# Kernel optimization log

Hardware: AMD Instinct MI355X
Metric: run time of the kernel (lower is better)

Reference implementation:

```python
import jax, jax.numpy as jnp
import numpy as np
import math

N_LAYERS = 6
F = 512   # num_feature
H = 8     # num_head
DH = F // H
V = 32000 # vocab size
B = 64
S = 512   # == PositionalEncoding max_len
EPS = 1e-5


def _make_pe(max_len, d_model):
    position = np.arange(max_len, dtype=np.float32)[:, None]
    div_term = np.exp(np.arange(0, d_model, 2, dtype=np.float32) * (-math.log(10000.0) / d_model))
    pe = np.zeros((max_len, d_model), dtype=np.float32)
    pe[:, 0::2] = np.sin(position * div_term)
    pe[:, 1::2] = np.cos(position * div_term)
    return jnp.asarray(pe)


def setup_inputs() -> dict:
    key = jax.random.key(0)
    ks = jax.random.split(key, 16)
    w = lambda k, shape, s=0.02: (jax.random.normal(k, shape, dtype=jnp.float32) * s)
    inp = {
        "text": jax.random.randint(ks[0], (B, S), 0, V),
        "emb": jax.random.normal(ks[1], (V, F), dtype=jnp.float32) * 0.25,
        "pe": _make_pe(S, F),
        # per-layer params stacked on leading N axis
        "Wq": w(ks[2], (N_LAYERS, F, F)), "bq": jnp.zeros((N_LAYERS, F), jnp.float32),
        "Wk": w(ks[3], (N_LAYERS, F, F)), "bk": jnp.zeros((N_LAYERS, F), jnp.float32),
        "Wv": w(ks[4], (N_LAYERS, F, F)), "bv": jnp.zeros((N_LAYERS, F), jnp.float32),
        "g1": jnp.ones((N_LAYERS, F), jnp.float32), "beta1": jnp.zeros((N_LAYERS, F), jnp.float32),
        "Wf": w(ks[5], (N_LAYERS, F, F)), "bf": jnp.zeros((N_LAYERS, F), jnp.float32),
        "g2": jnp.ones((N_LAYERS, F), jnp.float32), "beta2": jnp.zeros((N_LAYERS, F), jnp.float32),
    }
    return inp


def _layernorm(x, g, b):
    m = jnp.mean(x, axis=-1, keepdims=True)
    v = jnp.mean(jnp.square(x - m), axis=-1, keepdims=True)
    return (x - m) * jax.lax.rsqrt(v + EPS) * g + b


def _encoder_layer(x, Wq, bq, Wk, bk, Wv, bv, g1, beta1, Wf, bf, g2, beta2):
    Bz, Sz, Fz = x.shape
    q = (x @ Wq + bq).reshape(Bz, Sz, H, DH)
    k = (x @ Wk + bk).reshape(Bz, Sz, H, DH)
    v = (x @ Wv + bv).reshape(Bz, Sz, H, DH)
    # FAITHFUL to source bug: attention over HEADS per token, no 1/sqrt(d) scaling.
    score = jnp.einsum('bshd,bsgd->bshg', q, k)          # [B,S,H,H]
    weight = jax.nn.softmax(score, axis=-1)
    attn = jnp.einsum('bshg,bsgd->bshd', weight, v).reshape(Bz, Sz, Fz)
    x = _layernorm(attn + x, g1, beta1)
    x = _layernorm((x @ Wf + bf) + x, g2, beta2)
    return x


def reference(text, emb, pe, Wq, bq, Wk, bk, Wv, bv, g1, beta1, Wf, bf, g2, beta2):
    x = emb[text] + pe[None, :text.shape[1], :]  # embedding + pos-enc (dropout = eval identity)
    for i in range(N_LAYERS):
        x = _encoder_layer(x, Wq[i], bq[i], Wk[i], bk[i], Wv[i], bv[i],
                           g1[i], beta1[i], Wf[i], bf[i], g2[i], beta2[i])
    return x
```

## Files before the change

### kernel.cpp

```cpp
#include <hip/hip_runtime.h>
#include <stdint.h>

typedef unsigned short u16;
using frag8 = __attribute__((ext_vector_type(8))) short;
using f32x4 = __attribute__((ext_vector_type(4))) float;

#define NTOK 32768
#define FDIM 512

__device__ __forceinline__ float bflo(uint32_t p){ union{uint32_t u; float f;} v; v.u = p<<16; return v.f; }
__device__ __forceinline__ float bfhi(uint32_t p){ union{uint32_t u; float f;} v; v.u = p & 0xffff0000u; return v.f; }
__device__ __forceinline__ float bf1(u16 x){ union{uint32_t u; float f;} v; v.u = ((uint32_t)x)<<16; return v.f; }
__device__ __forceinline__ u16 f2bf(float f){
  union{float f; uint32_t u;} v; v.f = f;
  uint32_t u = v.u;
  u += 0x7fffu + ((u>>16)&1u);
  return (u16)(u>>16);
}

__device__ __forceinline__ void async16(const void* g, void* l){
  __builtin_amdgcn_global_load_lds((const __attribute__((address_space(1))) uint32_t*)g,
                                   (__attribute__((address_space(3))) uint32_t*)l, 16, 0, 0);
}

__global__ __launch_bounds__(256) void embed_kernel(const int* __restrict__ text,
    const float* __restrict__ emb, const float* __restrict__ pe,
    u16* __restrict__ xb, const int tok0){
  const int gid = blockIdx.x*256 + threadIdx.x;
  const int base = gid*4;
  const int tl = base >> 9;
  const int f  = base & 511;
  const int tg = tl + tok0;
  const int s  = tg & 511;
  const int tok = text[tg];
  const float4 e4 = *(const float4*)(emb + (size_t)tok*FDIM + f);
  const float4 p4 = *(const float4*)(pe  + (size_t)s*FDIM + f);
  ushort4 ob;
  ob.x = f2bf(e4.x + p4.x);
  ob.y = f2bf(e4.y + p4.y);
  ob.z = f2bf(e4.z + p4.z);
  ob.w = f2bf(e4.w + p4.w);
  *(ushort4*)(xb + base) = ob;
}

__global__ __launch_bounds__(256) void transpose_w(const float* __restrict__ Wq,
    const float* __restrict__ Wk, const float* __restrict__ Wv, const float* __restrict__ Wf,
    u16* __restrict__ WT){
  const int gid = blockIdx.x*256 + threadIdx.x;
  const int n   = gid & 2047;
  const int k8  = (gid>>11) & 63;
  const int lay = gid >> 17;
  const float* src; int col;
  if      (n <  512){ src = Wq; col = n;      }
  else if (n < 1024){ src = Wk; col = n-512;  }
  else if (n < 1536){ src = Wv; col = n-1024; }
  else              { src = Wf; col = n-1536; }
  src += (size_t)lay*FDIM*FDIM;
  u16 vals[8] __attribute__((aligned(16)));
  #pragma unroll
  for (int i=0;i<8;i++) vals[i] = f2bf(src[(size_t)(k8*8+i)*FDIM + col]);
  *(int4*)(WT + ((size_t)lay*2048 + n)*FDIM + k8*8) = *(const int4*)vals;
}

template<int MODE>
__global__ __launch_bounds__(256) void gemm_mfma(
    const u16* __restrict__ A, const u16* __restrict__ BT,
    const float* __restrict__ b0, const float* __restrict__ b1, const float* __restrict__ b2,
    const u16* __restrict__ resid, u16* __restrict__ C, int ldC){
  __shared__ __attribute__((aligned(16))) short As[128*32];
  __shared__ __attribute__((aligned(16))) short Bs[128*32];
  const int tid = threadIdx.x;
  const int w = tid>>6, l = tid&63;
  const int m0 = blockIdx.x*128;
  const int n0 = blockIdx.y*128;
  const int quad = l>>4, lm = l&15;
  const int wm = (w&1)*64, wn = (w>>1)*64;

  f32x4 acc[4][4];
  #pragma unroll
  for (int i=0;i<4;i++)
    #pragma unroll
    for (int j=0;j<4;j++){ f32x4 z = {0.f,0.f,0.f,0.f}; acc[i][j] = z; }

  const int cA = w*64 + l;
  const char* Ab = (const char*)(A  + (size_t)m0*FDIM) + (size_t)(cA>>2)*1024 + (cA&3)*16;
  const char* Bb = (const char*)(BT + (size_t)n0*FDIM) + (size_t)(cA>>2)*1024 + (cA&3)*16;
  char* ldsA = (char*)As + w*1024;
  char* ldsB = (char*)Bs + w*1024;

  for (int kb=0; kb<512; kb+=32){
    __syncthreads();
    async16(Ab + kb*2,         ldsA);
    async16(Ab + kb*2 + 65536, ldsA + 4096);
    async16(Bb + kb*2,         ldsB);
    async16(Bb + kb*2 + 65536, ldsB + 4096);
    __syncthreads();
    frag8 af[4], bfrg[4];
    #pragma unroll
    for (int i=0;i<4;i++) af[i]   = *(const frag8*)(As + (wm+i*16+lm)*32 + quad*8);
    #pragma unroll
    for (int j=0;j<4;j++) bfrg[j] = *(const frag8*)(Bs + (wn+j*16+lm)*32 + quad*8);
    #pragma unroll
    for (int i=0;i<4;i++)
      #pragma unroll
      for (int j=0;j<4;j++)
        acc[i][j] = __builtin_amdgcn_mfma_f32_16x16x32_bf16(af[i], bfrg[j], acc[i][j], 0,0,0);
  }

  float bias[4]; int cols[4];
  #pragma unroll
  for (int j=0;j<4;j++){
    const int c = n0 + wn + j*16 + lm;
    cols[j] = c;
    if (MODE==0) bias[j] = (c<512 ? b0[c] : (c<1024 ? b1[c-512] : b2[c-1024]));
    else         bias[j] = b0[c];
  }
  #pragma unroll
  for (int i=0;i<4;i++){
    const int rbase = m0 + wm + i*16 + quad*4;
    #pragma unroll
    for (int r=0;r<4;r++){
      const size_t row = (size_t)(rbase + r);
      #pragma unroll
      for (int j=0;j<4;j++){
        float v = acc[i][j][r] + bias[j];
        if (MODE==1) v += bf1(resid[row*FDIM + cols[j]]);
        C[row*(size_t)ldC + cols[j]] = f2bf(v);
      }
    }
  }
}

__global__ __launch_bounds__(256) void attn_ln1(const u16* __restrict__ qkvb,
    const u16* __restrict__ xb, const float* __restrict__ gam, const float* __restrict__ bet,
    u16* __restrict__ y1b){
  __shared__ __attribute__((aligned(16))) u16 sQ[4][1536];
  __shared__ float sWt[4][64];
  const int tid = threadIdx.x, w = tid>>6, l = tid&63;
  const int t = blockIdx.x*4 + w;
  {
    const int4* src = (const int4*)(qkvb + (size_t)t*1536);
    int4* dst = (int4*)(&sQ[w][0]);
    #pragma unroll
    for (int i=0;i<3;i++) dst[i*64 + l] = src[i*64 + l];
  }
  __syncthreads();
  const int h = l>>3, g = l&7;
  const u16* qrow = &sQ[w][h*64];
  const u16* krow = &sQ[w][512 + g*64];
  float sc = 0.f;
  const int dstart = (l&31)*2;
  #pragma unroll
  for (int i=0;i<32;i++){
    const int d = (dstart + 2*i) & 63;
    const uint32_t qp = *(const uint32_t*)(qrow + d);
    const uint32_t kp = *(const uint32_t*)(krow + d);
    sc += bflo(qp)*bflo(kp) + bfhi(qp)*bfhi(kp);
  }
  float mx = sc;
  mx = fmaxf(mx, __shfl_xor(mx,1));
  mx = fmaxf(mx, __shfl_xor(mx,2));
  mx = fmaxf(mx, __shfl_xor(mx,4));
  const float e = __expf(sc - mx);
  float ssum = e;
  ssum += __shfl_xor(ssum,1);
  ssum += __shfl_xor(ssum,2);
  ssum += __shfl_xor(ssum,4);
  sWt[w][l] = e / ssum;
  __syncthreads();
  float wt[8];
  #pragma unroll
  for (int gg=0;gg<8;gg++) wt[gg] = sWt[w][h*8+gg];
  float att[8] = {0,0,0,0,0,0,0,0};
  const int d0 = (l&7)*8;
  #pragma unroll
  for (int gg=0;gg<8;gg++){
    const int4 vv = *(const int4*)(&sQ[w][1024 + gg*64 + d0]);
    const uint32_t* vp = (const uint32_t*)&vv;
    #pragma unroll
    for (int p=0;p<4;p++){
      att[2*p]   += wt[gg]*bflo(vp[p]);
      att[2*p+1] += wt[gg]*bfhi(vp[p]);
    }
  }
  const size_t rb = (size_t)t*FDIM + l*8;
  const int4 xv = *(const int4*)(xb + rb);
  const uint32_t* xp = (const uint32_t*)&xv;
  float y[8]; float s1=0.f, s2=0.f;
  #pragma unroll
  for (int p=0;p<4;p++){
    y[2*p]   = att[2*p]   + bflo(xp[p]);
    y[2*p+1] = att[2*p+1] + bfhi(xp[p]);
  }
  #pragma unroll
  for (int j=0;j<8;j++){ s1 += y[j]; s2 += y[j]*y[j]; }
  #pragma unroll
  for (int off=1; off<64; off<<=1){ s1 += __shfl_xor(s1,off); s2 += __shfl_xor(s2,off); }
  const float mean = s1*(1.f/512.f);
  const float var  = s2*(1.f/512.f) - mean*mean;
  const float rstd = rsqrtf(var + 1e-5f);
  const float4 g0 = *(const float4*)(gam + l*8);
  const float4 g1v = *(const float4*)(gam + l*8 + 4);
  const float4 b0v = *(const float4*)(bet + l*8);
  const float4 b1v = *(const float4*)(bet + l*8 + 4);
  float of[8];
  of[0]=(y[0]-mean)*rstd*g0.x + b0v.x;
  of[1]=(y[1]-mean)*rstd*g0.y + b0v.y;
  of[2]=(y[2]-mean)*rstd*g0.z + b0v.z;
  of[3]=(y[3]-mean)*rstd*g0.w + b0v.w;
  of[4]=(y[4]-mean)*rstd*g1v.x + b1v.x;
  of[5]=(y[5]-mean)*rstd*g1v.y + b1v.y;
  of[6]=(y[6]-mean)*rstd*g1v.z + b1v.z;
  of[7]=(y[7]-mean)*rstd*g1v.w + b1v.w;
  u16 ob[8] __attribute__((aligned(16)));
  #pragma unroll
  for (int j=0;j<8;j++) ob[j] = f2bf(of[j]);
  *(int4*)(y1b + rb) = *(const int4*)ob;
}

__global__ __launch_bounds__(256) void ln2_kernel(const u16* __restrict__ z,
    const float* __restrict__ gam, const float* __restrict__ bet,
    u16* __restrict__ xb, float* __restrict__ outp, const int final_){
  const int tid = threadIdx.x, w = tid>>6, l = tid&63;
  const int t = blockIdx.x*4 + w;
  const size_t rb = (size_t)t*FDIM + l*8;
  const int4 zv = *(const int4*)(z + rb);
  const uint32_t* zp = (const uint32_t*)&zv;
  float y[8];
  #pragma unroll
  for (int p=0;p<4;p++){ y[2*p]=bflo(zp[p]); y[2*p+1]=bfhi(zp[p]); }
  float s1=0.f, s2=0.f;
  #pragma unroll
  for (int j=0;j<8;j++){ s1+=y[j]; s2+=y[j]*y[j]; }
  #pragma unroll
  for (int off=1; off<64; off<<=1){ s1 += __shfl_xor(s1,off); s2 += __shfl_xor(s2,off); }
  const float mean = s1*(1.f/512.f);
  const float var  = s2*(1.f/512.f) - mean*mean;
  const float rstd = rsqrtf(var + 1e-5f);
  const float4 g0 = *(const float4*)(gam + l*8);
  const float4 g1v = *(const float4*)(gam + l*8 + 4);
  const float4 b0v = *(const float4*)(bet + l*8);
  const float4 b1v = *(const float4*)(bet + l*8 + 4);
  float of[8];
  of[0]=(y[0]-mean)*rstd*g0.x + b0v.x;
  of[1]=(y[1]-mean)*rstd*g0.y + b0v.y;
  of[2]=(y[2]-mean)*rstd*g0.z + b0v.z;
  of[3]=(y[3]-mean)*rstd*g0.w + b0v.w;
  of[4]=(y[4]-mean)*rstd*g1v.x + b1v.x;
  of[5]=(y[5]-mean)*rstd*g1v.y + b1v.y;
  of[6]=(y[6]-mean)*rstd*g1v.z + b1v.z;
  of[7]=(y[7]-mean)*rstd*g1v.w + b1v.w;
  if (final_){
    float4 o0; o0.x=of[0]; o0.y=of[1]; o0.z=of[2]; o0.w=of[3];
    float4 o1; o1.x=of[4]; o1.y=of[5]; o1.z=of[6]; o1.w=of[7];
    *(float4*)(outp + rb) = o0;
    *(float4*)(outp + rb + 4) = o1;
  } else {
    u16 ob[8] __attribute__((aligned(16)));
    #pragma unroll
    for (int j=0;j<8;j++) ob[j] = f2bf(of[j]);
    *(int4*)(xb + rb) = *(const int4*)ob;
  }
}

extern "C" void kernel_launch(void* const* d_in, const int* in_sizes, int n_in,
                              void* d_out, int out_size, void* d_ws, size_t ws_size,
                              hipStream_t stream){
  const int*   text = (const int*)d_in[0];
  const float* emb = (const float*)d_in[1];
  const float* pe  = (const float*)d_in[2];
  const float* Wq  = (const float*)d_in[3];
  const float* bq  = (const float*)d_in[4];
  const float* Wk  = (const float*)d_in[5];
  const float* bk  = (const float*)d_in[6];
  const float* Wv  = (const float*)d_in[7];
  const float* bv  = (const float*)d_in[8];
  const float* g1  = (const float*)d_in[9];
  const float* be1 = (const float*)d_in[10];
  const float* Wf  = (const float*)d_in[11];
  const float* bf_ = (const float*)d_in[12];
  const float* g2  = (const float*)d_in[13];
  const float* be2 = (const float*)d_in[14];
  float* outp = (float*)d_out;

  const size_t wtB = (size_t)6*2048*512*2;
  int T = NTOK;
  while (T > 2048 && wtB + (size_t)T*5120 > ws_size) T >>= 1;

  char* ws = (char*)d_ws;
  u16*   WT  = (u16*)ws;
  char*  act = ws + wtB;
  u16*   xb  = (u16*)act;
  u16*   y1b = (u16*)(act + (size_t)T*1024);
  u16*   qkv = (u16*)(act + (size_t)T*2048);
  u16*   zb  = qkv;

  hipLaunchKernelGGL(transpose_w, dim3(3072), dim3(256), 0, stream, Wq, Wk, Wv, Wf, WT);

  const int chunks = NTOK / T;
  for (int c = 0; c < chunks; c++){
    const int tok0 = c*T;
    hipLaunchKernelGGL(embed_kernel, dim3(T/2), dim3(256), 0, stream, text, emb, pe, xb, tok0);
    for (int lay=0; lay<6; lay++){
      const u16* WTl = WT + (size_t)lay*2048*FDIM;
      hipLaunchKernelGGL((gemm_mfma<0>), dim3(T/128, 12), dim3(256), 0, stream,
          xb, WTl, bq + lay*FDIM, bk + lay*FDIM, bv + lay*FDIM, (const u16*)nullptr, qkv, 1536);
      hipLaunchKernelGGL(attn_ln1, dim3(T/4), dim3(256), 0, stream,
          qkv, xb, g1 + lay*FDIM, be1 + lay*FDIM, y1b);
      hipLaunchKernelGGL((gemm_mfma<1>), dim3(T/128, 4), dim3(256), 0, stream,
          y1b, WTl + (size_t)1536*FDIM, bf_ + lay*FDIM, (const float*)nullptr, (const float*)nullptr,
          y1b, zb, 512);
      hipLaunchKernelGGL(ln2_kernel, dim3(T/4), dim3(256), 0, stream,
          zb, g2 + lay*FDIM, be2 + lay*FDIM, xb, outp + (size_t)tok0*FDIM, (lay==5)?1:0);
    }
  }
}
```

Measured before the change: 1.051 ms.

## Replace 128x128 GEMM with 256x256-tile, 4-stage async-pipelined MFMA kernel

Measured after the change: 969.0 us. 7.8% less time.

```diff
diff --git a/kernel.cpp b/kernel.cpp
--- a/kernel.cpp
+++ b/kernel.cpp
@@ -63,69 +63,109 @@
 }
 
 template<int MODE>
-__global__ __launch_bounds__(256) void gemm_mfma(
+__global__ __launch_bounds__(512, 2) void gemm256(
     const u16* __restrict__ A, const u16* __restrict__ BT,
     const float* __restrict__ b0, const float* __restrict__ b1, const float* __restrict__ b2,
-    const u16* __restrict__ resid, u16* __restrict__ C, int ldC){
-  __shared__ __attribute__((aligned(16))) short As[128*32];
-  __shared__ __attribute__((aligned(16))) short Bs[128*32];
+    const u16* __restrict__ resid, u16* __restrict__ C, const int ldC, const int NB){
+  __shared__ __attribute__((aligned(16))) short As[4*256*32];
+  __shared__ __attribute__((aligned(16))) short Bs[4*256*32];
+  const int nwg = gridDim.x;
+  const int orig = blockIdx.x;
+  const int wg = ((nwg & 7) == 0) ? ((orig & 7)*(nwg >> 3) + (orig >> 3)) : orig;
+  const int nblk = wg % NB, mblk = wg / NB;
+  const int m0 = mblk << 8, n0 = nblk << 8;
   const int tid = threadIdx.x;
-  const int w = tid>>6, l = tid&63;
-  const int m0 = blockIdx.x*128;
-  const int n0 = blockIdx.y*128;
-  const int quad = l>>4, lm = l&15;
-  const int wm = (w&1)*64, wn = (w>>1)*64;
-
-  f32x4 acc[4][4];
-  #pragma unroll
-  for (int i=0;i<4;i++)
+  const int wid = tid >> 6, l = tid & 63;
+  const int lm = l & 15, quad = l >> 4;
+
+  const int srow = wid*16 + (l >> 2);
+  const int sch  = (l & 3) ^ ((l >> 3) & 3);
+  const char* Asrc0 = (const char*)A  + ((size_t)(m0 + srow))*1024 + sch*16;
+  const char* Asrc1 = Asrc0 + 128*1024;
+  const char* Bsrc0 = (const char*)BT + ((size_t)(n0 + srow))*1024 + sch*16;
+  const char* Bsrc1 = Bsrc0 + 128*1024;
+  char* ldsAw = (char*)As + wid*1024;
+  char* ldsBw = (char*)Bs + wid*1024;
+
+  f32x4 acc[8][4];
+  #pragma unroll
+  for (int i=0;i<8;i++)
     #pragma unroll
     for (int j=0;j<4;j++){ f32x4 z = {0.f,0.f,0.f,0.f}; acc[i][j] = z; }
 
-  const int cA = w*64 + l;
-  const char* Ab = (const char*)(A  + (size_t)m0*FDIM) + (size_t)(cA>>2)*1024 + (cA&3)*16;
-  const char* Bb = (const char*)(BT + (size_t)n0*FDIM) + (size_t)(cA>>2)*1024 + (cA&3)*16;
-  char* ldsA = (char*)As + w*1024;
-  char* ldsB = (char*)Bs + w*1024;
-
-  for (int kb=0; kb<512; kb+=32){
-    __syncthreads();
-    async16(Ab + kb*2,         ldsA);
-    async16(Ab + kb*2 + 65536, ldsA + 4096);
-    async16(Bb + kb*2,         ldsB);
-    async16(Bb + kb*2 + 65536, ldsB + 4096);
-    __syncthreads();
-    frag8 af[4], bfrg[4];
-    #pragma unroll
-    for (int i=0;i<4;i++) af[i]   = *(const frag8*)(As + (wm+i*16+lm)*32 + quad*8);
-    #pragma unroll
-    for (int j=0;j<4;j++) bfrg[j] = *(const frag8*)(Bs + (wn+j*16+lm)*32 + quad*8);
-    #pragma unroll
-    for (int i=0;i<4;i++)
+  const int rsel = quad ^ ((lm >> 1) & 3);
+  const int aB = ((wid>>2)*128 + lm)*32 + rsel*8;
+  const int bB = ((wid&3)*64  + lm)*32 + rsel*8;
+
+  #pragma unroll
+  for (int kt=0; kt<3; kt++){
+    async16(Asrc0 + kt*64, ldsAw + kt*16384);
+    async16(Asrc1 + kt*64, ldsAw + kt*16384 + 8192);
+    async16(Bsrc0 + kt*64, ldsBw + kt*16384);
+    async16(Bsrc1 + kt*64, ldsBw + kt*16384 + 8192);
+  }
+
+  for (int t=0; t<16; ++t){
+    if (t < 14)       asm volatile("s_waitcnt vmcnt(8)" ::: "memory");
+    else if (t == 14) asm volatile("s_waitcnt vmcnt(4)" ::: "memory");
+    else              asm volatile("s_waitcnt vmcnt(0)" ::: "memory");
+    __builtin_amdgcn_s_barrier();
+    asm volatile("" ::: "memory");
+    const int slot = t & 3;
+    const short* sA = As + slot*8192;
+    const short* sB = Bs + slot*8192;
+    frag8 af[4], bf[4], ag[4];
+    #pragma unroll
+    for (int mi=0; mi<4; mi++) af[mi] = *(const frag8*)(sA + aB + mi*512);
+    #pragma unroll
+    for (int nj=0; nj<4; nj++) bf[nj] = *(const frag8*)(sB + bB + nj*512);
+    if (t < 13){
+      const int s3 = (t+3) & 3, off = (t+3)*64;
+      async16(Asrc0 + off, ldsAw + s3*16384);
+      async16(Asrc1 + off, ldsAw + s3*16384 + 8192);
+    }
+    __builtin_amdgcn_s_setprio(1);
+    #pragma unroll
+    for (int mi=0; mi<4; mi++)
       #pragma unroll
-      for (int j=0;j<4;j++)
-        acc[i][j] = __builtin_amdgcn_mfma_f32_16x16x32_bf16(af[i], bfrg[j], acc[i][j], 0,0,0);
+      for (int nj=0; nj<4; nj++)
+        acc[mi][nj] = __builtin_amdgcn_mfma_f32_16x16x32_bf16(af[mi], bf[nj], acc[mi][nj], 0,0,0);
+    __builtin_amdgcn_s_setprio(0);
+    #pragma unroll
+    for (int mi=0; mi<4; mi++) ag[mi] = *(const frag8*)(sA + aB + 2048 + mi*512);
+    if (t < 13){
+      const int s3 = (t+3) & 3, off = (t+3)*64;
+      async16(Bsrc0 + off, ldsBw + s3*16384);
+      async16(Bsrc1 + off, ldsBw + s3*16384 + 8192);
+    }
+    __builtin_amdgcn_s_setprio(1);
+    #pragma unroll
+    for (int mi=0; mi<4; mi++)
+      #pragma unroll
+      for (int nj=0; nj<4; nj++)
+        acc[4+mi][nj] = __builtin_amdgcn_mfma_f32_16x16x32_bf16(ag[mi], bf[nj], acc[4+mi][nj], 0,0,0);
+    __builtin_amdgcn_s_setprio(0);
   }
 
   float bias[4]; int cols[4];
   #pragma unroll
-  for (int j=0;j<4;j++){
-    const int c = n0 + wn + j*16 + lm;
-    cols[j] = c;
-    if (MODE==0) bias[j] = (c<512 ? b0[c] : (c<1024 ? b1[c-512] : b2[c-1024]));
-    else         bias[j] = b0[c];
-  }
-  #pragma unroll
-  for (int i=0;i<4;i++){
-    const int rbase = m0 + wm + i*16 + quad*4;
+  for (int nj=0;nj<4;nj++){
+    const int c = n0 + (wid&3)*64 + nj*16 + lm;
+    cols[nj] = c;
+    if (MODE==0) bias[nj] = (c<512 ? b0[c] : (c<1024 ? b1[c-512] : b2[c-1024]));
+    else         bias[nj] = b0[c];
+  }
+  #pragma unroll
+  for (int mi=0; mi<8; mi++){
+    const int rbase = m0 + (wid>>2)*128 + mi*16 + quad*4;
     #pragma unroll
     for (int r=0;r<4;r++){
       const size_t row = (size_t)(rbase + r);
       #pragma unroll
-      for (int j=0;j<4;j++){
-        float v = acc[i][j][r] + bias[j];
-        if (MODE==1) v += bf1(resid[row*FDIM + cols[j]]);
-        C[row*(size_t)ldC + cols[j]] = f2bf(v);
+      for (int nj=0;nj<4;nj++){
+        float v = acc[mi][nj][r] + bias[nj];
+        if (MODE==1) v += bf1(resid[row*FDIM + cols[nj]]);
+        C[row*(size_t)ldC + cols[nj]] = f2bf(v);
       }
     }
   }
@@ -303,13 +343,13 @@
     hipLaunchKernelGGL(embed_kernel, dim3(T/2), dim3(256), 0, stream, text, emb, pe, xb, tok0);
     for (int lay=0; lay<6; lay++){
       const u16* WTl = WT + (size_t)lay*2048*FDIM;
-      hipLaunchKernelGGL((gemm_mfma<0>), dim3(T/128, 12), dim3(256), 0, stream,
-          xb, WTl, bq + lay*FDIM, bk + lay*FDIM, bv + lay*FDIM, (const u16*)nullptr, qkv, 1536);
+      hipLaunchKernelGGL((gemm256<0>), dim3((T/256)*6), dim3(512), 0, stream,
+          xb, WTl, bq + lay*FDIM, bk + lay*FDIM, bv + lay*FDIM, (const u16*)nullptr, qkv, 1536, 6);
       hipLaunchKernelGGL(attn_ln1, dim3(T/4), dim3(256), 0, stream,
           qkv, xb, g1 + lay*FDIM, be1 + lay*FDIM, y1b);
-      hipLaunchKernelGGL((gemm_mfma<1>), dim3(T/128, 4), dim3(256), 0, stream,
+      hipLaunchKernelGGL((gemm256<1>), dim3((T/256)*2), dim3(512), 0, stream,
           y1b, WTl + (size_t)1536*FDIM, bf_ + lay*FDIM, (const float*)nullptr, (const float*)nullptr,
-          y1b, zb, 512);
+          y1b, zb, 512, 2);
       hipLaunchKernelGGL(ln2_kernel, dim3(T/4), dim3(256), 0, stream,
           zb, g2 + lay*FDIM, be2 + lay*FDIM, xb, outp + (size_t)tok0*FDIM, (lay==5)?1:0);
     }
```
